# Kernel tuning notes

Hardware: AMD Instinct MI355X
Metric: run time of the kernel (lower is better)

Reference implementation:

```python
import jax, jax.numpy as jnp
import numpy as np

ALPHA = 1.0
EPS = 1e-8

def setup_inputs() -> dict:
    key = jax.random.key(0)
    k1, k2, k3 = jax.random.split(key, 3)
    B, L, S, H, E, D = 4, 2048, 2048, 8, 64, 64
    queries = jax.random.normal(k1, (B, L, H, E), dtype=jnp.float32)
    keys = jax.random.normal(k2, (B, S, H, E), dtype=jnp.float32)
    values = jax.random.normal(k3, (B, S, H, D), dtype=jnp.float32)
    return {"queries": queries, "keys": keys, "values": values}

def reference(queries, keys, values):
    E = queries.shape[3]
    scale = 1.0 / jnp.sqrt(jnp.asarray(E, queries.dtype))
    # dot_product: [B,H,L,S]
    dot = jnp.einsum('blhe,bshe->bhls', queries, keys)
    q_norm2 = jnp.sum(queries ** 2, axis=-1).transpose(0, 2, 1)[..., :, None]  # [B,H,L,1]
    k_norm2 = jnp.sum(keys ** 2, axis=-1).transpose(0, 2, 1)[..., None, :]     # [B,H,1,S]
    wedge2 = jax.nn.relu(q_norm2 * k_norm2 - dot ** 2)
    wedge = jnp.sqrt(wedge2 + EPS)
    scores = ((1.0 - ALPHA) * dot + ALPHA * wedge) * scale
    A = jax.nn.softmax(scores, axis=-1)  # dropout in eval mode = identity
    out = jnp.einsum('bhls,bshd->blhd', A, values)
    return out
```

## Files before the change

kernel.cpp:

```cpp
#include <hip/hip_runtime.h>

typedef __attribute__((ext_vector_type(4))) float f32x4;
typedef __attribute__((ext_vector_type(4))) float float4v;
typedef __attribute__((ext_vector_type(8))) short bf16x8;
typedef __attribute__((ext_vector_type(8))) unsigned short ushort8;

#define DEVI static __device__ __forceinline__

namespace {
constexpr int kL = 2048, kS = 2048, kH = 8;
constexpr int QB = 64, KVB = 64, NKT = kS / KVB;
constexpr float kC = 0.18033688f;
constexpr int KTILE = 8448;
constexpr int VTILE = 8192;
constexpr int KBH = 32 * KTILE;
constexpr int VBH = 32 * VTILE;
constexpr int LBUF = KTILE + VTILE;
}

DEVI int swz(int byteoff) { return byteoff ^ (((byteoff >> 7) & 7) << 4); }

DEVI unsigned cvtpk(float lo, float hi) {
  unsigned r;
  asm("v_cvt_pk_bf16_f32 %0, %1, %2" : "=v"(r) : "v"(lo), "v"(hi));
  return r;
}

__global__ __launch_bounds__(256) void prep_k(const float* __restrict__ Kg,
                                              char* __restrict__ Kb) {
  const int chunk = (int)blockIdx.x * 256 + (int)threadIdx.x;
  const int tile = chunk >> 9;
  const int i = chunk & 511;
  const int bh = tile >> 5, kt = tile & 31;
  const int b = bh >> 3, h = bh & 7;
  const int row = i >> 3;
  const int colsel = (i & 7) ^ (row & 7);
  const int s = kt * 64 + row;
  const float* src = Kg + (((size_t)b * kS + s) * kH + h) * 64 + colsel * 8;
  float4v v0 = *(const float4v*)(src);
  float4v v1 = *(const float4v*)(src + 4);
  float pn = v0.x*v0.x + v0.y*v0.y + v0.z*v0.z + v0.w*v0.w
           + v1.x*v1.x + v1.y*v1.y + v1.z*v1.z + v1.w*v1.w;
  union { unsigned w[4]; ushort8 u; } o;
  o.w[0] = cvtpk(v0.x, v0.y); o.w[1] = cvtpk(v0.z, v0.w);
  o.w[2] = cvtpk(v1.x, v1.y); o.w[3] = cvtpk(v1.z, v1.w);
  char* tb = Kb + (size_t)tile * KTILE;
  *(ushort8*)(tb + i * 16) = o.u;
  pn += __shfl_xor(pn, 1);
  pn += __shfl_xor(pn, 2);
  pn += __shfl_xor(pn, 4);
  if ((i & 7) == 0) *(float*)(tb + 8192 + row * 4) = pn;
}

__global__ __launch_bounds__(256) void prep_v(const float* __restrict__ Vg,
                                              char* __restrict__ Vt) {
  __shared__ char tile[64 * 128];
  const int t = (int)threadIdx.x;
  const int bid = (int)blockIdx.x;
  const int st = bid & 31, bh = bid >> 5;
  const int b = bh >> 3, h = bh & 7;
  {
    const int sl = t >> 2, c0 = (t & 3) * 16;
    const float* src = Vg + (((size_t)b * kS + st * 64 + sl) * kH + h) * 64 + c0;
    float4v v0 = *(const float4v*)(src);
    float4v v1 = *(const float4v*)(src + 4);
    float4v v2 = *(const float4v*)(src + 8);
    float4v v3 = *(const float4v*)(src + 12);
    union { unsigned w[4]; ushort8 u; } t0, t1;
    t0.w[0] = cvtpk(v0.x, v0.y); t0.w[1] = cvtpk(v0.z, v0.w);
    t0.w[2] = cvtpk(v1.x, v1.y); t0.w[3] = cvtpk(v1.z, v1.w);
    t1.w[0] = cvtpk(v2.x, v2.y); t1.w[1] = cvtpk(v2.z, v2.w);
    t1.w[2] = cvtpk(v3.x, v3.y); t1.w[3] = cvtpk(v3.z, v3.w);
    *(ushort8*)(tile + swz(sl * 128 + c0 * 2)) = t0.u;
    *(ushort8*)(tile + swz(sl * 128 + c0 * 2 + 16)) = t1.u;
  }
  __syncthreads();
  char* dst = Vt + (size_t)bid * VTILE;
#pragma unroll
  for (int cc = 0; cc < 2; ++cc) {
    const int i = t * 2 + cc;
    const int z = swz(i * 16);
    const int d = z >> 7;
    const int k0 = ((z >> 4) & 7) * 8;
    union { unsigned short s[8]; ushort8 u; } o;
#pragma unroll
    for (int j = 0; j < 8; ++j) {
      const int k = k0 + j;
      const int sig = (((k >> 5) * 2 + ((k & 7) >> 2)) << 4) |
                      (((k >> 3) & 3) << 2) | (k & 3);
      o.s[j] = *(const unsigned short*)(tile + swz(sig * 128 + d * 2));
    }
    *(ushort8*)(dst + i * 16) = o.u;
  }
}

__global__ __launch_bounds__(256, 4) void geo_attn_kernel(
    const float* __restrict__ Qg, const char* __restrict__ Kb,
    const char* __restrict__ Vt, float* __restrict__ Og) {
  __shared__ char lds[2 * LBUF];

  const int t = (int)threadIdx.x;
  const int wv = t >> 6, lane = t & 63, gg = lane >> 4, cl = lane & 15;
  const int n = (int)blockIdx.x;
  const int bh = (n & 7) * 4 + ((n >> 3) & 3);
  const int l0 = (n >> 5) * QB;
  const int b = bh >> 3, h = bh & 7;

  const int q = l0 + wv * 16 + cl;
  const float* qp = Qg + (((size_t)b * kL + q) * kH + h) * 64;
  float4v x0 = *(const float4v*)(qp + gg * 8);
  float4v x1 = *(const float4v*)(qp + gg * 8 + 4);
  float4v x2 = *(const float4v*)(qp + gg * 8 + 32);
  float4v x3 = *(const float4v*)(qp + gg * 8 + 36);
  x0 *= kC; x1 *= kC; x2 *= kC; x3 *= kC;
  float pn = 0.f;
#pragma unroll
  for (int j = 0; j < 4; ++j) {
    pn = fmaf(x0[j], x0[j], pn); pn = fmaf(x1[j], x1[j], pn);
    pn = fmaf(x2[j], x2[j], pn); pn = fmaf(x3[j], x3[j], pn);
  }
  union frag { bf16x8 v; unsigned w[4]; };
  frag qb0, qb1;
  qb0.w[0] = cvtpk(x0.x, x0.y); qb0.w[1] = cvtpk(x0.z, x0.w);
  qb0.w[2] = cvtpk(x1.x, x1.y); qb0.w[3] = cvtpk(x1.z, x1.w);
  qb1.w[0] = cvtpk(x2.x, x2.y); qb1.w[1] = cvtpk(x2.z, x2.w);
  qb1.w[2] = cvtpk(x3.x, x3.y); qb1.w[3] = cvtpk(x3.z, x3.w);
  pn += __shfl_xor(pn, 16);
  pn += __shfl_xor(pn, 32);
  const float qn2 = pn;

  frag vone;
  vone.w[0] = vone.w[1] = vone.w[2] = vone.w[3] = 0x3F803F80u;

  const char* pA = lds + ((cl * 128 + gg * 16) ^ ((cl & 7) << 4));
  const char* pB = lds + ((cl * 128 + gg * 16 + 64) ^ ((cl & 7) << 4));
  const char* pT = lds + gg * 16;

  const bool isK = (wv < 2);
  const char* gp = (isK ? Kb + (size_t)bh * KBH : Vt + (size_t)bh * VBH)
                   + (wv & 1) * 4096 + lane * 16;
  const int gstride = isK ? KTILE : VTILE;
  const char* gt = Kb + (size_t)bh * KBH + 8192 + lane * 4;
  const int ldsoff = isK ? (wv & 1) * 4096 : KTILE + (wv & 1) * 4096;
  char* const sd0 = lds + ldsoff;
  char* const sd1 = lds + LBUF + ldsoff;
  char* const st0 = lds + 8192 + lane * 4;
  char* const st1 = lds + LBUF + 8192 + lane * 4;

#define STAGE(SD, ST) do { \
    __builtin_amdgcn_global_load_lds((__attribute__((address_space(1))) void*)(gp),        (__attribute__((address_space(3))) void*)(SD),        16, 0, 0); \
    __builtin_amdgcn_global_load_lds((__attribute__((address_space(1))) void*)(gp + 1024), (__attribute__((address_space(3))) void*)((SD) + 1024), 16, 0, 0); \
    __builtin_amdgcn_global_load_lds((__attribute__((address_space(1))) void*)(gp + 2048), (__attribute__((address_space(3))) void*)((SD) + 2048), 16, 0, 0); \
    __builtin_amdgcn_global_load_lds((__attribute__((address_space(1))) void*)(gp + 3072), (__attribute__((address_space(3))) void*)((SD) + 3072), 16, 0, 0); \
    if (wv == 0) \
      __builtin_amdgcn_global_load_lds((__attribute__((address_space(1))) void*)(gt), (__attribute__((address_space(3))) void*)(ST), 4, 0, 0); \
    gp += gstride; gt += KTILE; \
  } while (0)

  f32x4 oacc[4];
#pragma unroll
  for (int dt = 0; dt < 4; ++dt) oacc[dt] = (f32x4){0.f, 0.f, 0.f, 0.f};
  f32x4 lacc = (f32x4){0.f, 0.f, 0.f, 0.f};

#define BODY(BO) do { \
    float4v kn2v[4]; \
    _Pragma("unroll") for (int nt = 0; nt < 4; ++nt) \
      kn2v[nt] = *(const float4v*)(pT + (BO) + 8192 + nt * 64); \
    f32x4 dacc[4]; \
    __builtin_amdgcn_s_setprio(1); \
    _Pragma("unroll") for (int nt = 0; nt < 4; ++nt) { \
      bf16x8 ka0 = *(const bf16x8*)(pA + (BO) + nt * 2048); \
      bf16x8 ka1 = *(const bf16x8*)(pB + (BO) + nt * 2048); \
      f32x4 acc = {0.f, 0.f, 0.f, 0.f}; \
      acc = __builtin_amdgcn_mfma_f32_16x16x32_bf16(ka0, qb0.v, acc, 0, 0, 0); \
      acc = __builtin_amdgcn_mfma_f32_16x16x32_bf16(ka1, qb1.v, acc, 0, 0, 0); \
      dacc[nt] = acc; } \
    __builtin_amdgcn_s_setprio(0); \
    bf16x8 vb0[4], vb1[4]; \
    _Pragma("unroll") for (int dt = 0; dt < 4; ++dt) { \
      vb0[dt] = *(const bf16x8*)(pA + (BO) + KTILE + dt * 2048); \
      vb1[dt] = *(const bf16x8*)(pB + (BO) + KTILE + dt * 2048); } \
    float sc[4][4]; \
    _Pragma("unroll") for (int nt = 0; nt < 2; ++nt) \
      _Pragma("unroll") for (int r = 0; r < 4; ++r) { \
        const float d = dacc[nt][r]; \
        const float w2 = fmaf(-d, d, qn2 * kn2v[nt][r]); \
        sc[nt][r] = __builtin_amdgcn_exp2f(__builtin_amdgcn_sqrtf(fabsf(w2))); } \
    frag pa0; \
    pa0.w[0] = cvtpk(sc[0][0], sc[0][1]); pa0.w[1] = cvtpk(sc[0][2], sc[0][3]); \
    pa0.w[2] = cvtpk(sc[1][0], sc[1][1]); pa0.w[3] = cvtpk(sc[1][2], sc[1][3]); \
    __builtin_amdgcn_s_setprio(1); \
    _Pragma("unroll") for (int dt = 0; dt < 4; ++dt) \
      oacc[dt] = __builtin_amdgcn_mfma_f32_16x16x32_bf16(pa0.v, vb0[dt], oacc[dt], 0, 0, 0); \
    lacc = __builtin_amdgcn_mfma_f32_16x16x32_bf16(pa0.v, vone.v, lacc, 0, 0, 0); \
    __builtin_amdgcn_s_setprio(0); \
    _Pragma("unroll") for (int nt = 2; nt < 4; ++nt) \
      _Pragma("unroll") for (int r = 0; r < 4; ++r) { \
        const float d = dacc[nt][r]; \
        const float w2 = fmaf(-d, d, qn2 * kn2v[nt][r]); \
        sc[nt][r] = __builtin_amdgcn_exp2f(__builtin_amdgcn_sqrtf(fabsf(w2))); } \
    frag pa1; \
    pa1.w[0] = cvtpk(sc[2][0], sc[2][1]); pa1.w[1] = cvtpk(sc[2][2], sc[2][3]); \
    pa1.w[2] = cvtpk(sc[3][0], sc[3][1]); pa1.w[3] = cvtpk(sc[3][2], sc[3][3]); \
    __builtin_amdgcn_s_setprio(1); \
    _Pragma("unroll") for (int dt = 0; dt < 4; ++dt) \
      oacc[dt] = __builtin_amdgcn_mfma_f32_16x16x32_bf16(pa1.v, vb1[dt], oacc[dt], 0, 0, 0); \
    lacc = __builtin_amdgcn_mfma_f32_16x16x32_bf16(pa1.v, vone.v, lacc, 0, 0, 0); \
    __builtin_amdgcn_s_setprio(0); \
  } while (0)

  STAGE(sd0, st0);
  __syncthreads();

#pragma unroll 1
  for (int it = 0; it < NKT / 2; ++it) {
    STAGE(sd1, st1);
    BODY(0);
    __syncthreads();
    if (it + 1 < NKT / 2) STAGE(sd0, st0);
    BODY(LBUF);
    __syncthreads();
  }
#undef STAGE
#undef BODY

#pragma unroll
  for (int r = 0; r < 4; ++r) {
    const int l = l0 + wv * 16 + gg * 4 + r;
    const float inv = 1.f / lacc[r];
    float* op = Og + (((size_t)b * kL + l) * kH + h) * 64;
#pragma unroll
    for (int dt = 0; dt < 4; ++dt)
      op[dt * 16 + cl] = oacc[dt][r] * inv;
  }
}

extern "C" void kernel_launch(void* const* d_in, const int* in_sizes, int n_in,
                              void* d_out, int out_size, void* d_ws, size_t ws_size,
                              hipStream_t stream) {
  const float* Qg = (const float*)d_in[0];
  const float* Kg = (const float*)d_in[1];
  const float* Vg = (const float*)d_in[2];
  float* Og = (float*)d_out;
  char* Kb = (char*)d_ws;
  char* Vt = (char*)d_ws + (size_t)1024 * KTILE;
  prep_k<<<2048, 256, 0, stream>>>(Kg, Kb);
  prep_v<<<1024, 256, 0, stream>>>(Vg, Vt);
  geo_attn_kernel<<<dim3(1024), dim3(256), 0, stream>>>(Qg, Kb, Vt, Og);
}
```

Baseline: 69.17 us.

## Load key norms directly from global memory and pack qn2*kn2 multiplies

Key squared norms move into a separate global array. Each lane now reads them straight from global memory instead of staging them through LDS with an extra 4-byte global_load_lds per tile. The K and V tiles are simplified to a uniform 8 KB, and the qn2*kn2 products are computed with packed v_pk_mul_f32. The loop also issues the final stage unconditionally, which over-reads past the last tile into adjacent workspace, and the norm loads now add global-memory latency inside the loop body.

```diff
diff --git a/kernel.cpp b/kernel.cpp
--- a/kernel.cpp
+++ b/kernel.cpp
@@ -1,5 +1,6 @@
 #include <hip/hip_runtime.h>
 
+typedef __attribute__((ext_vector_type(2))) float f32x2;
 typedef __attribute__((ext_vector_type(4))) float f32x4;
 typedef __attribute__((ext_vector_type(4))) float float4v;
 typedef __attribute__((ext_vector_type(8))) short bf16x8;
@@ -11,11 +12,9 @@
 constexpr int kL = 2048, kS = 2048, kH = 8;
 constexpr int QB = 64, KVB = 64, NKT = kS / KVB;
 constexpr float kC = 0.18033688f;
-constexpr int KTILE = 8448;
-constexpr int VTILE = 8192;
-constexpr int KBH = 32 * KTILE;
-constexpr int VBH = 32 * VTILE;
-constexpr int LBUF = KTILE + VTILE;
+constexpr int TILE = 8192;
+constexpr int BH = 32 * TILE;
+constexpr int LBUF = 2 * TILE;
 }
 
 DEVI int swz(int byteoff) { return byteoff ^ (((byteoff >> 7) & 7) << 4); }
@@ -26,8 +25,15 @@
   return r;
 }
 
+DEVI f32x2 pkmul(f32x2 a, f32x2 b) {
+  f32x2 r;
+  asm("v_pk_mul_f32 %0, %1, %2" : "=v"(r) : "v"(a), "v"(b));
+  return r;
+}
+
 __global__ __launch_bounds__(256) void prep_k(const float* __restrict__ Kg,
-                                              char* __restrict__ Kb) {
+                                              char* __restrict__ Kb,
+                                              float* __restrict__ kn2g) {
   const int chunk = (int)blockIdx.x * 256 + (int)threadIdx.x;
   const int tile = chunk >> 9;
   const int i = chunk & 511;
@@ -44,12 +50,11 @@
   union { unsigned w[4]; ushort8 u; } o;
   o.w[0] = cvtpk(v0.x, v0.y); o.w[1] = cvtpk(v0.z, v0.w);
   o.w[2] = cvtpk(v1.x, v1.y); o.w[3] = cvtpk(v1.z, v1.w);
-  char* tb = Kb + (size_t)tile * KTILE;
-  *(ushort8*)(tb + i * 16) = o.u;
+  *(ushort8*)(Kb + (size_t)tile * TILE + i * 16) = o.u;
   pn += __shfl_xor(pn, 1);
   pn += __shfl_xor(pn, 2);
   pn += __shfl_xor(pn, 4);
-  if ((i & 7) == 0) *(float*)(tb + 8192 + row * 4) = pn;
+  if ((i & 7) == 0) kn2g[tile * 64 + row] = pn;
 }
 
 __global__ __launch_bounds__(256) void prep_v(const float* __restrict__ Vg,
@@ -75,7 +80,7 @@
     *(ushort8*)(tile + swz(sl * 128 + c0 * 2 + 16)) = t1.u;
   }
   __syncthreads();
-  char* dst = Vt + (size_t)bid * VTILE;
+  char* dst = Vt + (size_t)bid * TILE;
 #pragma unroll
   for (int cc = 0; cc < 2; ++cc) {
     const int i = t * 2 + cc;
@@ -96,7 +101,8 @@
 
 __global__ __launch_bounds__(256, 4) void geo_attn_kernel(
     const float* __restrict__ Qg, const char* __restrict__ Kb,
-    const char* __restrict__ Vt, float* __restrict__ Og) {
+    const char* __restrict__ Vt, const float* __restrict__ kn2g,
+    float* __restrict__ Og) {
   __shared__ char lds[2 * LBUF];
 
   const int t = (int)threadIdx.x;
@@ -127,34 +133,27 @@
   qb1.w[2] = cvtpk(x3.x, x3.y); qb1.w[3] = cvtpk(x3.z, x3.w);
   pn += __shfl_xor(pn, 16);
   pn += __shfl_xor(pn, 32);
-  const float qn2 = pn;
+  const f32x2 qn2d = {pn, pn};
 
   frag vone;
   vone.w[0] = vone.w[1] = vone.w[2] = vone.w[3] = 0x3F803F80u;
 
   const char* pA = lds + ((cl * 128 + gg * 16) ^ ((cl & 7) << 4));
   const char* pB = lds + ((cl * 128 + gg * 16 + 64) ^ ((cl & 7) << 4));
-  const char* pT = lds + gg * 16;
 
   const bool isK = (wv < 2);
-  const char* gp = (isK ? Kb + (size_t)bh * KBH : Vt + (size_t)bh * VBH)
-                   + (wv & 1) * 4096 + lane * 16;
-  const int gstride = isK ? KTILE : VTILE;
-  const char* gt = Kb + (size_t)bh * KBH + 8192 + lane * 4;
-  const int ldsoff = isK ? (wv & 1) * 4096 : KTILE + (wv & 1) * 4096;
+  const char* gp = (isK ? Kb : Vt) + (size_t)bh * BH + (wv & 1) * 4096 + lane * 16;
+  const int ldsoff = (isK ? 0 : TILE) + (wv & 1) * 4096;
   char* const sd0 = lds + ldsoff;
   char* const sd1 = lds + LBUF + ldsoff;
-  char* const st0 = lds + 8192 + lane * 4;
-  char* const st1 = lds + LBUF + 8192 + lane * 4;
-
-#define STAGE(SD, ST) do { \
+  const float* kn2p = kn2g + bh * 2048 + gg * 4;
+
+#define STAGE(SD) do { \
     __builtin_amdgcn_global_load_lds((__attribute__((address_space(1))) void*)(gp),        (__attribute__((address_space(3))) void*)(SD),        16, 0, 0); \
     __builtin_amdgcn_global_load_lds((__attribute__((address_space(1))) void*)(gp + 1024), (__attribute__((address_space(3))) void*)((SD) + 1024), 16, 0, 0); \
     __builtin_amdgcn_global_load_lds((__attribute__((address_space(1))) void*)(gp + 2048), (__attribute__((address_space(3))) void*)((SD) + 2048), 16, 0, 0); \
     __builtin_amdgcn_global_load_lds((__attribute__((address_space(1))) void*)(gp + 3072), (__attribute__((address_space(3))) void*)((SD) + 3072), 16, 0, 0); \
-    if (wv == 0) \
-      __builtin_amdgcn_global_load_lds((__attribute__((address_space(1))) void*)(gt), (__attribute__((address_space(3))) void*)(ST), 4, 0, 0); \
-    gp += gstride; gt += KTILE; \
+    gp += TILE; \
   } while (0)
 
   f32x4 oacc[4];
@@ -162,10 +161,10 @@
   for (int dt = 0; dt < 4; ++dt) oacc[dt] = (f32x4){0.f, 0.f, 0.f, 0.f};
   f32x4 lacc = (f32x4){0.f, 0.f, 0.f, 0.f};
 
-#define BODY(BO) do { \
+#define BODY(BO, KF) do { \
     float4v kn2v[4]; \
     _Pragma("unroll") for (int nt = 0; nt < 4; ++nt) \
-      kn2v[nt] = *(const float4v*)(pT + (BO) + 8192 + nt * 64); \
+      kn2v[nt] = *(const float4v*)(kn2p + (KF) + nt * 16); \
     f32x4 dacc[4]; \
     __builtin_amdgcn_s_setprio(1); \
     _Pragma("unroll") for (int nt = 0; nt < 4; ++nt) { \
@@ -176,15 +175,22 @@
       acc = __builtin_amdgcn_mfma_f32_16x16x32_bf16(ka1, qb1.v, acc, 0, 0, 0); \
       dacc[nt] = acc; } \
     __builtin_amdgcn_s_setprio(0); \
+    f32x2 qk2lo[4], qk2hi[4]; \
+    _Pragma("unroll") for (int nt = 0; nt < 4; ++nt) { \
+      const f32x2 klo = {kn2v[nt][0], kn2v[nt][1]}; \
+      const f32x2 khi = {kn2v[nt][2], kn2v[nt][3]}; \
+      qk2lo[nt] = pkmul(qn2d, klo); \
+      qk2hi[nt] = pkmul(qn2d, khi); } \
     bf16x8 vb0[4], vb1[4]; \
     _Pragma("unroll") for (int dt = 0; dt < 4; ++dt) { \
-      vb0[dt] = *(const bf16x8*)(pA + (BO) + KTILE + dt * 2048); \
-      vb1[dt] = *(const bf16x8*)(pB + (BO) + KTILE + dt * 2048); } \
+      vb0[dt] = *(const bf16x8*)(pA + (BO) + TILE + dt * 2048); \
+      vb1[dt] = *(const bf16x8*)(pB + (BO) + TILE + dt * 2048); } \
     float sc[4][4]; \
     _Pragma("unroll") for (int nt = 0; nt < 2; ++nt) \
       _Pragma("unroll") for (int r = 0; r < 4; ++r) { \
         const float d = dacc[nt][r]; \
-        const float w2 = fmaf(-d, d, qn2 * kn2v[nt][r]); \
+        const float qk2 = (r < 2) ? qk2lo[nt][r] : qk2hi[nt][r - 2]; \
+        const float w2 = fmaf(-d, d, qk2); \
         sc[nt][r] = __builtin_amdgcn_exp2f(__builtin_amdgcn_sqrtf(fabsf(w2))); } \
     frag pa0; \
     pa0.w[0] = cvtpk(sc[0][0], sc[0][1]); pa0.w[1] = cvtpk(sc[0][2], sc[0][3]); \
@@ -197,7 +203,8 @@
     _Pragma("unroll") for (int nt = 2; nt < 4; ++nt) \
       _Pragma("unroll") for (int r = 0; r < 4; ++r) { \
         const float d = dacc[nt][r]; \
-        const float w2 = fmaf(-d, d, qn2 * kn2v[nt][r]); \
+        const float qk2 = (r < 2) ? qk2lo[nt][r] : qk2hi[nt][r - 2]; \
+        const float w2 = fmaf(-d, d, qk2); \
         sc[nt][r] = __builtin_amdgcn_exp2f(__builtin_amdgcn_sqrtf(fabsf(w2))); } \
     frag pa1; \
     pa1.w[0] = cvtpk(sc[2][0], sc[2][1]); pa1.w[1] = cvtpk(sc[2][2], sc[2][3]); \
@@ -209,17 +216,18 @@
     __builtin_amdgcn_s_setprio(0); \
   } while (0)
 
-  STAGE(sd0, st0);
+  STAGE(sd0);
   __syncthreads();
 
 #pragma unroll 1
   for (int it = 0; it < NKT / 2; ++it) {
-    STAGE(sd1, st1);
-    BODY(0);
+    STAGE(sd1);
+    BODY(0, 0);
     __syncthreads();
-    if (it + 1 < NKT / 2) STAGE(sd0, st0);
-    BODY(LBUF);
+    STAGE(sd0);
+    BODY(LBUF, 64);
     __syncthreads();
+    kn2p += 128;
   }
 #undef STAGE
 #undef BODY
@@ -243,8 +251,9 @@
   const float* Vg = (const float*)d_in[2];
   float* Og = (float*)d_out;
   char* Kb = (char*)d_ws;
-  char* Vt = (char*)d_ws + (size_t)1024 * KTILE;
-  prep_k<<<2048, 256, 0, stream>>>(Kg, Kb);
+  char* Vt = (char*)d_ws + ((size_t)8 << 20);
+  float* kn2g = (float*)((char*)d_ws + ((size_t)16 << 20));
+  prep_k<<<2048, 256, 0, stream>>>(Kg, Kb, kn2g);
   prep_v<<<1024, 256, 0, stream>>>(Vg, Vt);
-  geo_attn_kernel<<<dim3(1024), dim3(256), 0, stream>>>(Qg, Kb, Vt, Og);
-}
+  geo_attn_kernel<<<dim3(1024), dim3(256), 0, stream>>>(Qg, Kb, Vt, kn2g, Og);
+}
```

After: 71.80 us. +3.8%, slower.
